# Kernel tuning notes

Measured on AMD Instinct MI355X. Metric: run time of the kernel, lower is better.

The kernel has to match this reference:

```python
import jax, jax.numpy as jnp
import numpy as np

N, E, IN_DIM, HID, OUT = 50000, 800000, 128, 64, 64


def setup_inputs() -> dict:
    key = jax.random.key(0)
    ks = jax.random.split(key, 8)
    x = jax.random.normal(ks[0], (N, IN_DIM), dtype=jnp.float32)
    edge_index = jax.random.randint(ks[1], (2, E), 0, N, dtype=jnp.int64)
    # Glorot-style init like PyG GCNConv linear; bias zeros-init equivalent -> small randn for generality
    def glorot(k, fan_in, fan_out):
        s = (6.0 / (fan_in + fan_out)) ** 0.5
        return jax.random.uniform(k, (fan_in, fan_out), jnp.float32, -s, s)
    W1 = glorot(ks[2], IN_DIM, HID)
    b1 = jnp.zeros((HID,), jnp.float32)
    W2 = glorot(ks[3], HID, HID)
    b2 = jnp.zeros((HID,), jnp.float32)
    W3 = glorot(ks[4], HID, OUT)
    b3 = jnpp = jnp.zeros((OUT,), jnp.float32)
    return {"x": x, "edge_index": edge_index, "W1": W1, "b1": b1,
            "W2": W2, "b2": b2, "W3": W3, "b3": b3}


def _gcn_norm(edge_index, num_nodes):
    # PyG gcn_norm with add_self_loops=True, edge_weight=1:
    # A_hat = A + I; deg over target column; norm = d^-1/2[src] * d^-1/2[dst]
    loops = jnp.arange(num_nodes, dtype=edge_index.dtype)
    src = jnp.concatenate([edge_index[0], loops])
    dst = jnp.concatenate([edge_index[1], loops])
    ones = jnp.ones(src.shape[0], dtype=jnp.float32)
    deg = jax.ops.segment_sum(ones, dst, num_segments=num_nodes)
    dinv = jnp.where(deg > 0, jax.lax.rsqrt(deg), 0.0)
    norm = dinv[src] * dinv[dst]  # [E+N]
    return src, dst, norm


def _conv(h, src, dst, norm, W, b, num_nodes):
    h = h @ W                         # [N, F_out] dense transform first (PyG order)
    msg = norm[:, None] * h[src]      # gather + degree-normalize, [E+N, F_out]
    out = jax.ops.segment_sum(msg, dst, num_segments=num_nodes)  # scatter-add
    return out + b


def reference(x, edge_index, W1, b1, W2, b2, W3, b3):
    num_nodes = x.shape[0]
    src, dst, norm = _gcn_norm(edge_index, num_nodes)
    h = _conv(x, src, dst, norm, W1, b1, num_nodes)
    h = jax.nn.relu(h)  # dropout is identity in eval / p=0
    h = _conv(h, src, dst, norm, W2, b2, num_nodes)
    h = jax.nn.relu(h)
    h = _conv(h, src, dst, norm, W3, b3, num_nodes)
    return h
```

## Files before the change

### kernel.cpp

```cpp
#include <hip/hip_runtime.h>


#define FD 64
#define P1CHUNK 4096
#define CAP 8192

typedef unsigned short ushort_t;
typedef unsigned int uint_t;

__device__ __forceinline__ ushort_t f2bf(float f) {
    uint_t u = __float_as_uint(f);
    u = (u + 0x7fffu + ((u >> 16) & 1u)) >> 16;
    return (ushort_t)u;
}
__device__ __forceinline__ uint_t pack2bf(float f0, float f1) {
    return (uint_t)f2bf(f0) | ((uint_t)f2bf(f1) << 16);
}

__global__ __launch_bounds__(256) void scan_buckets(const int* __restrict__ cnt,
                                                    int* __restrict__ bucketBase,
                                                    int* __restrict__ rowptr,
                                                    int NB, int N, int E) {
    __shared__ int wsum[4];
    int tid = threadIdx.x, lane = tid & 63, wv = tid >> 6;
    int v = (tid < NB) ? min(cnt[tid], CAP) : 0;
    int x = v;
    for (int off = 1; off < 64; off <<= 1) {
        int t = __shfl_up(x, off, 64);
        if (lane >= off) x += t;
    }
    if (lane == 63) wsum[wv] = x;
    __syncthreads();
    int wex = 0;
    for (int i = 0; i < wv; ++i) wex += wsum[i];
    int excl = wex + x - v;
    if (tid < NB) bucketBase[tid] = excl;
    if (tid == 0) { bucketBase[NB] = E; rowptr[N] = E; }
}

template <int K, bool SCALE>
__device__ __forceinline__ void gemm_body(int bid, const float* __restrict__ x,
                                          const float* __restrict__ W,
                                          const float* __restrict__ dinv,
                                          ushort_t* __restrict__ out, int nrows,
                                          float* Xs ) {
    constexpr int KP = K + 4;
    constexpr int NC = K / 4;
    constexpr int YP = 68;
    const int tid = threadIdx.x;
    const int lane = tid & 63;
    const int rowBase = bid * 64;

    for (int idx = tid; idx < 64 * NC; idx += 256) {
        int row = idx / NC, kc = idx % NC;
        int r = rowBase + row;
        float4 v = (r < nrows) ? *(const float4*)(x + (size_t)r * K + kc * 4)
                               : make_float4(0.f, 0.f, 0.f, 0.f);
        *(float4*)(&Xs[row * KP + kc * 4]) = v;
    }
    __syncthreads();

    const int c0 = __builtin_amdgcn_readfirstlane((tid >> 6) * 16);
    float acc[16];
#pragma unroll
    for (int i = 0; i < 16; ++i) acc[i] = 0.f;
    const float* Xrow = &Xs[lane * KP];

#pragma unroll 4
    for (int k = 0; k < K; k += 4) {
        float4 xv = *(const float4*)(Xrow + k);
        const float* wp = W + (size_t)k * FD + c0;
#pragma unroll
        for (int ci = 0; ci < 16; ++ci) {
            acc[ci] = fmaf(xv.x, wp[ci], acc[ci]);
            acc[ci] = fmaf(xv.y, wp[FD + ci], acc[ci]);
            acc[ci] = fmaf(xv.z, wp[2 * FD + ci], acc[ci]);
            acc[ci] = fmaf(xv.w, wp[3 * FD + ci], acc[ci]);
        }
    }

    int r = rowBase + lane;
    float di = 1.0f;
    if (SCALE) di = (r < nrows) ? dinv[r] : 0.f;
    __syncthreads();
    float* Ys = Xs;
#pragma unroll
    for (int ci = 0; ci < 16; ++ci) Ys[lane * YP + c0 + ci] = acc[ci] * di;
    __syncthreads();

    for (int i = tid; i < 64 * 16; i += 256) {
        int row = i >> 4, seg = i & 15;
        int rr = rowBase + row;
        if (rr < nrows) {
            float4 v = *(const float4*)(&Ys[row * YP + seg * 4]);
            uint2 p;
            p.x = pack2bf(v.x, v.y);
            p.y = pack2bf(v.z, v.w);
            *(uint2*)(out + (size_t)rr * FD + seg * 4) = p;
        }
    }
}

template <int K>
__global__ __launch_bounds__(256) void gemm_kernel(const float* __restrict__ x,
                                                   const float* __restrict__ W,
                                                   const float* __restrict__ dinv,
                                                   ushort_t* __restrict__ out, int nrows) {
    __shared__ float Xs[64 * (K + 4)];
    gemm_body<K, true>(blockIdx.x, x, W, dinv, out, nrows, Xs);
}

__global__ __launch_bounds__(256) void fused_gemm1_scatter(
    const float* __restrict__ x, const float* __restrict__ W1,
    ushort_t* __restrict__ hB, int nrows,
    const int* __restrict__ src, const int* __restrict__ dst,
    int* __restrict__ cnt, uint_t* __restrict__ staged, int E, int nGemmBlk) {
    __shared__ float Xs[64 * 132];
    int bid = blockIdx.x;
    if (bid < nGemmBlk) {
        gemm_body<128, false>(bid, x, W1, nullptr, hB, nrows, Xs);
        return;
    }
    int* hist = (int*)Xs;
    int* gbase = hist + 256;
    int tid = threadIdx.x;
    hist[tid] = 0;
    __syncthreads();
    int base = (bid - nGemmBlk) * P1CHUNK;
#pragma unroll
    for (int k = 0; k < 16; ++k) {
        int e = base + k * 256 + tid;
        if (e < E) atomicAdd(&hist[dst[e] >> 8], 1);
    }
    __syncthreads();
    int h = hist[tid];
    gbase[tid] = h ? atomicAdd(&cnt[tid], h) : 0;
    hist[tid] = 0;
    __syncthreads();
#pragma unroll
    for (int k = 0; k < 16; ++k) {
        int e = base + k * 256 + tid;
        if (e < E) {
            int s = src[e], d = dst[e];
            int b = d >> 8;
            int r = atomicAdd(&hist[b], 1);
            int p = gbase[b] + r;
            if (p < CAP) staged[(size_t)b * CAP + p] = (uint_t)s | ((uint_t)(d & 255) << 16);
        }
    }
}

__global__ __launch_bounds__(256) void bucket_sort(const uint_t* __restrict__ staged,
                                                   const int* __restrict__ cnt,
                                                   const int* __restrict__ bucketBase,
                                                   int* __restrict__ rowptr,
                                                   float* __restrict__ dinv,
                                                   ushort_t* __restrict__ csr,
                                                   ushort_t* __restrict__ hB,
                                                   int* __restrict__ dhist, int N) {
    __shared__ int ncnt[256];
    __shared__ int nrp[256];
    __shared__ int wsum[4];
    __shared__ float sdinv[256];
    __shared__ int dh[64];
    int tid = threadIdx.x, lane = tid & 63, wv = tid >> 6;
    int b = blockIdx.x;
    int gbeg = bucketBase[b];
    int cntE = min(cnt[b], CAP);
    const uint_t* sb = staged + (size_t)b * CAP;
    ncnt[tid] = 0;
    if (tid < 64) dh[tid] = 0;
    __syncthreads();
    for (int i = tid; i < cntE; i += 256)
        atomicAdd(&ncnt[(sb[i] >> 16) & 255], 1);
    __syncthreads();
    int v = ncnt[tid];
    int x = v;
    for (int off = 1; off < 64; off <<= 1) {
        int t = __shfl_up(x, off, 64);
        if (lane >= off) x += t;
    }
    if (lane == 63) wsum[wv] = x;
    __syncthreads();
    int wex = 0;
    for (int i = 0; i < wv; ++i) wex += wsum[i];
    int excl = wex + x - v;
    nrp[tid] = excl;
    int node = b * 256 + tid;
    float di = rsqrtf((float)(v + 1));
    sdinv[tid] = di;
    if (node < N) {
        dinv[node] = di;
        atomicAdd(&dh[min(v, 63)], 1);
    }
    if (node <= N) rowptr[node] = gbeg + excl;
    ncnt[tid] = 0;
    __syncthreads();
    if (tid < 64 && dh[tid]) atomicAdd(&dhist[tid], dh[tid]);
    for (int i = tid; i < cntE; i += 256) {
        uint_t p = sb[i];
        int dl = (p >> 16) & 255;
        int lofs = atomicAdd(&ncnt[dl], 1);
        csr[(size_t)gbeg + nrp[dl] + lofs] = (ushort_t)(p & 0xffffu);
    }
    uint2* hB2 = (uint2*)hB;
    for (int idx = tid; idx < 256 * 16; idx += 256) {
        int row = idx >> 4, c = idx & 15;
        int g = b * 256 + row;
        if (g < N) {
            float d = sdinv[row];
            uint2 u = hB2[(size_t)g * 16 + c];
            float f0 = __uint_as_float(u.x << 16) * d;
            float f1 = __uint_as_float(u.x & 0xffff0000u) * d;
            float f2 = __uint_as_float(u.y << 16) * d;
            float f3 = __uint_as_float(u.y & 0xffff0000u) * d;
            uint2 o;
            o.x = pack2bf(f0, f1);
            o.y = pack2bf(f2, f3);
            hB2[(size_t)g * 16 + c] = o;
        }
    }
}

__global__ void deg_scan(const int* __restrict__ dhist, int* __restrict__ dcursor) {
    int lane = threadIdx.x;
    int v = dhist[lane];
    int x = v;
    for (int off = 1; off < 64; off <<= 1) {
        int t = __shfl_up(x, off, 64);
        if (lane >= off) x += t;
    }
    dcursor[lane] = x - v;
}

__global__ __launch_bounds__(256) void deg_scatter(const int* __restrict__ rowptr,
                                                   int* __restrict__ dcursor,
                                                   int* __restrict__ perm, int N) {
    __shared__ int h[64];
    __shared__ int gb[64];
    int tid = threadIdx.x;
    if (tid < 64) h[tid] = 0;
    __syncthreads();
    int node = blockIdx.x * 256 + tid;
    bool val = node < N;
    int d = 0;
    if (val) {
        d = min(rowptr[node + 1] - rowptr[node], 63);
        atomicAdd(&h[d], 1);
    }
    __syncthreads();
    if (tid < 64) {
        int c = h[tid];
        gb[tid] = c ? atomicAdd(&dcursor[tid], c) : 0;
        h[tid] = 0;
    }
    __syncthreads();
    if (val) {
        int r = atomicAdd(&h[d], 1);
        perm[gb[d] + r] = node;
    }
}

__device__ __forceinline__ void bf8_acc(uint4 a, float* acc) {
    acc[0] += __uint_as_float(a.x << 16);
    acc[1] += __uint_as_float(a.x & 0xffff0000u);
    acc[2] += __uint_as_float(a.y << 16);
    acc[3] += __uint_as_float(a.y & 0xffff0000u);
    acc[4] += __uint_as_float(a.z << 16);
    acc[5] += __uint_as_float(a.z & 0xffff0000u);
    acc[6] += __uint_as_float(a.w << 16);
    acc[7] += __uint_as_float(a.w & 0xffff0000u);
}

template <bool RELU>
__global__ __launch_bounds__(256) void agg_fused(
    const int* __restrict__ rowptr, const ushort_t* __restrict__ csr,
    const int* __restrict__ perm,
    const float* __restrict__ dinv, const ushort_t* __restrict__ h,
    const float* __restrict__ b, float* __restrict__ out, int N) {
    int wid = (blockIdx.x * blockDim.x + threadIdx.x) >> 6;
    int lane = threadIdx.x & 63;
    int l8 = lane & 7;
    int widx = wid * 8 + (lane >> 3);
    bool valid = widx < N;
    int nd = perm[valid ? widx : 0];
    int beg = rowptr[nd];
    int end = valid ? rowptr[nd + 1] : beg;
    const uint4* __restrict__ h4 = (const uint4*)h;
    float acc[8];
#pragma unroll
    for (int k = 0; k < 8; ++k) acc[k] = 0.f;
    bf8_acc(h4[(size_t)nd * 8 + l8], acc);
    int j = beg;
    for (; j + 3 < end; j += 4) {
        int s0 = csr[j], s1 = csr[j + 1], s2 = csr[j + 2], s3 = csr[j + 3];
        uint4 a0 = h4[(size_t)s0 * 8 + l8];
        uint4 a1 = h4[(size_t)s1 * 8 + l8];
        uint4 a2 = h4[(size_t)s2 * 8 + l8];
        uint4 a3 = h4[(size_t)s3 * 8 + l8];
        bf8_acc(a0, acc); bf8_acc(a1, acc); bf8_acc(a2, acc); bf8_acc(a3, acc);
    }
    for (; j < end; ++j) bf8_acc(h4[(size_t)csr[j] * 8 + l8], acc);

    float di = dinv[nd];
    float4 b0 = *(const float4*)(b + l8 * 8);
    float4 b1 = *(const float4*)(b + l8 * 8 + 4);
    float4 v0, v1;
    v0.x = fmaf(di, acc[0], b0.x); v0.y = fmaf(di, acc[1], b0.y);
    v0.z = fmaf(di, acc[2], b0.z); v0.w = fmaf(di, acc[3], b0.w);
    v1.x = fmaf(di, acc[4], b1.x); v1.y = fmaf(di, acc[5], b1.y);
    v1.z = fmaf(di, acc[6], b1.z); v1.w = fmaf(di, acc[7], b1.w);
    if (RELU) {
        v0.x = fmaxf(v0.x, 0.f); v0.y = fmaxf(v0.y, 0.f);
        v0.z = fmaxf(v0.z, 0.f); v0.w = fmaxf(v0.w, 0.f);
        v1.x = fmaxf(v1.x, 0.f); v1.y = fmaxf(v1.y, 0.f);
        v1.z = fmaxf(v1.z, 0.f); v1.w = fmaxf(v1.w, 0.f);
    }
    if (valid) {
        float* op = out + (size_t)nd * FD + l8 * 8;
        *(float4*)op = v0;
        *(float4*)(op + 4) = v1;
    }
}

extern "C" void kernel_launch(void* const* d_in, const int* in_sizes, int n_in,
                              void* d_out, int out_size, void* d_ws, size_t ws_size,
                              hipStream_t stream) {
    const float* x  = (const float*)d_in[0];
    const int*   ei = (const int*)d_in[1];
    const float* W1 = (const float*)d_in[2];
    const float* b1 = (const float*)d_in[3];
    const float* W2 = (const float*)d_in[4];
    const float* b2 = (const float*)d_in[5];
    const float* W3 = (const float*)d_in[6];
    const float* b3 = (const float*)d_in[7];
    float* out = (float*)d_out;

    const int N = in_sizes[0] / 128;
    const int E = in_sizes[1] / 2;
    const int* src = ei;
    const int* dst = ei + E;
    const int NB = (N + 255) / 256;

    float*    f1     = (float*)d_ws;
    ushort_t* hB     = (ushort_t*)(f1 + (size_t)N * FD);
    float*    dinv   = (float*)(hB + (size_t)N * FD);
    int*      rowptr = (int*)(dinv + N);
    int*   cnt       = rowptr + N + 1;
    int*   dhist     = cnt + NB;
    int*   dcursor   = dhist + 64;
    int*   bucketBase= dcursor + 64;
    int*   perm      = bucketBase + NB + 1;
    uint_t*   staged = (uint_t*)(perm + N);
    ushort_t* csr    = (ushort_t*)(staged + (size_t)NB * CAP);

    const int nSctBlk = (E + P1CHUNK - 1) / P1CHUNK;
    const int nGemmBlk = (N + 63) / 64;
    dim3 blk(256);
    dim3 gGemm(nGemmBlk);
    dim3 gAgg((N + 31) / 32);

    hipMemsetAsync(cnt, 0, (size_t)(NB + 64) * sizeof(int), stream);
    fused_gemm1_scatter<<<dim3(nGemmBlk + nSctBlk), blk, 0, stream>>>(
        x, W1, hB, N, src, dst, cnt, staged, E, nGemmBlk);
    scan_buckets<<<dim3(1), blk, 0, stream>>>(cnt, bucketBase, rowptr, NB, N, E);
    bucket_sort<<<dim3(NB), blk, 0, stream>>>(staged, cnt, bucketBase, rowptr, dinv,
                                              csr, hB, dhist, N);
    deg_scan<<<dim3(1), dim3(64), 0, stream>>>(dhist, dcursor);
    deg_scatter<<<dim3(NB), blk, 0, stream>>>(rowptr, dcursor, perm, N);

    agg_fused<true><<<gAgg, blk, 0, stream>>>(rowptr, csr, perm, dinv, hB, b1, f1, N);

    gemm_kernel<64><<<gGemm, blk, 0, stream>>>(f1, W2, dinv, hB, N);
    agg_fused<true><<<gAgg, blk, 0, stream>>>(rowptr, csr, perm, dinv, hB, b2, f1, N);

    gemm_kernel<64><<<gGemm, blk, 0, stream>>>(f1, W3, dinv, hB, N);
    agg_fused<false><<<gAgg, blk, 0, stream>>>(rowptr, csr, perm, dinv, hB, b3, out, N);
}
```

Before: 141.1 us.

## Fuse layer aggregation with next-layer dense transform into single kernel

Aggregation for layers 1 and 2 now runs in one 512-thread kernel per layer. It applies bias and ReLU, stages the 64 aggregated rows in shared memory, multiplies them by the next weight matrix, scales by dinv, and writes bf16 output directly. This removes the fp32 intermediate round-trip through global memory and two separate GEMM launches. Rows in a block follow the degree-sorted permutation, so the output writes are scattered, and ping-pong bf16 buffers replace the fp32 workspace.

```diff
diff --git a/kernel.cpp b/kernel.cpp
--- a/kernel.cpp
+++ b/kernel.cpp
@@ -38,15 +38,11 @@
     if (tid == 0) { bucketBase[NB] = E; rowptr[N] = E; }
 }
 
-template <int K, bool SCALE>
-__device__ __forceinline__ void gemm_body(int bid, const float* __restrict__ x,
-                                          const float* __restrict__ W,
-                                          const float* __restrict__ dinv,
-                                          ushort_t* __restrict__ out, int nrows,
-                                          float* Xs ) {
-    constexpr int KP = K + 4;
-    constexpr int NC = K / 4;
-    constexpr int YP = 68;
+__device__ __forceinline__ void gemm_body128(int bid, const float* __restrict__ x,
+                                             const float* __restrict__ W,
+                                             ushort_t* __restrict__ out, int nrows,
+                                             float* Xs ) {
+    constexpr int K = 128, KP = 132, NC = 32, YP = 68;
     const int tid = threadIdx.x;
     const int lane = tid & 63;
     const int rowBase = bid * 64;
@@ -78,14 +74,10 @@
             acc[ci] = fmaf(xv.w, wp[3 * FD + ci], acc[ci]);
         }
     }
-
-    int r = rowBase + lane;
-    float di = 1.0f;
-    if (SCALE) di = (r < nrows) ? dinv[r] : 0.f;
     __syncthreads();
     float* Ys = Xs;
 #pragma unroll
-    for (int ci = 0; ci < 16; ++ci) Ys[lane * YP + c0 + ci] = acc[ci] * di;
+    for (int ci = 0; ci < 16; ++ci) Ys[lane * YP + c0 + ci] = acc[ci];
     __syncthreads();
 
     for (int i = tid; i < 64 * 16; i += 256) {
@@ -101,15 +93,6 @@
     }
 }
 
-template <int K>
-__global__ __launch_bounds__(256) void gemm_kernel(const float* __restrict__ x,
-                                                   const float* __restrict__ W,
-                                                   const float* __restrict__ dinv,
-                                                   ushort_t* __restrict__ out, int nrows) {
-    __shared__ float Xs[64 * (K + 4)];
-    gemm_body<K, true>(blockIdx.x, x, W, dinv, out, nrows, Xs);
-}
-
 __global__ __launch_bounds__(256) void fused_gemm1_scatter(
     const float* __restrict__ x, const float* __restrict__ W1,
     ushort_t* __restrict__ hB, int nrows,
@@ -118,7 +101,7 @@
     __shared__ float Xs[64 * 132];
     int bid = blockIdx.x;
     if (bid < nGemmBlk) {
-        gemm_body<128, false>(bid, x, W1, nullptr, hB, nrows, Xs);
+        gemm_body128(bid, x, W1, hB, nrows, Xs);
         return;
     }
     int* hist = (int*)Xs;
@@ -272,8 +255,84 @@
     acc[7] += __uint_as_float(a.w & 0xffff0000u);
 }
 
-template <bool RELU>
-__global__ __launch_bounds__(256) void agg_fused(
+__global__ __launch_bounds__(512) void agg_gemm(
+    const int* __restrict__ rowptr, const ushort_t* __restrict__ csr,
+    const int* __restrict__ perm, const float* __restrict__ dinv,
+    const ushort_t* __restrict__ hIn, const float* __restrict__ bias,
+    const float* __restrict__ W, ushort_t* __restrict__ hOut, int N) {
+    __shared__ float Xs[64 * 65];
+    __shared__ float sdi[64];
+    __shared__ int snode[64];
+    const int tid = threadIdx.x;
+    const int wave = tid >> 6, lane = tid & 63;
+    const int l8 = lane & 7;
+    const int nodeSlot = wave * 8 + (lane >> 3);
+    int widx = blockIdx.x * 64 + nodeSlot;
+    bool valid = widx < N;
+    int nd = perm[valid ? widx : 0];
+    int beg = rowptr[nd];
+    int end = valid ? rowptr[nd + 1] : beg;
+    const uint4* __restrict__ h4 = (const uint4*)hIn;
+    float acc[8];
+#pragma unroll
+    for (int k = 0; k < 8; ++k) acc[k] = 0.f;
+    bf8_acc(h4[(size_t)nd * 8 + l8], acc);
+    int j = beg;
+    for (; j + 3 < end; j += 4) {
+        int s0 = csr[j], s1 = csr[j + 1], s2 = csr[j + 2], s3 = csr[j + 3];
+        uint4 a0 = h4[(size_t)s0 * 8 + l8];
+        uint4 a1 = h4[(size_t)s1 * 8 + l8];
+        uint4 a2 = h4[(size_t)s2 * 8 + l8];
+        uint4 a3 = h4[(size_t)s3 * 8 + l8];
+        bf8_acc(a0, acc); bf8_acc(a1, acc); bf8_acc(a2, acc); bf8_acc(a3, acc);
+    }
+    for (; j < end; ++j) bf8_acc(h4[(size_t)csr[j] * 8 + l8], acc);
+
+    float di = dinv[nd];
+    const float* bp = bias + l8 * 8;
+    if (l8 == 0) { sdi[nodeSlot] = di; snode[nodeSlot] = valid ? nd : -1; }
+#pragma unroll
+    for (int k = 0; k < 8; ++k) {
+        float v = fmaf(di, acc[k], bp[k]);
+        v = fmaxf(v, 0.f);
+        Xs[nodeSlot * 65 + l8 * 8 + k] = v;
+    }
+    __syncthreads();
+
+    const int c0 = __builtin_amdgcn_readfirstlane(wave * 8);
+    float a2[8];
+#pragma unroll
+    for (int i = 0; i < 8; ++i) a2[i] = 0.f;
+    const float* Xrow = &Xs[lane * 65];
+#pragma unroll 4
+    for (int k = 0; k < 64; ++k) {
+        float xv = Xrow[k];
+        const float* wp = W + k * FD + c0;
+#pragma unroll
+        for (int ci = 0; ci < 8; ++ci) a2[ci] = fmaf(xv, wp[ci], a2[ci]);
+    }
+    float dro = sdi[lane];
+    int gnode = snode[lane];
+    (void)gnode;
+    __syncthreads();
+#pragma unroll
+    for (int ci = 0; ci < 8; ++ci) Xs[lane * 65 + c0 + ci] = a2[ci] * dro;
+    __syncthreads();
+
+    for (int i = tid; i < 64 * 16; i += 512) {
+        int row = i >> 4, seg = i & 15;
+        int g = snode[row];
+        if (g >= 0) {
+            const float* yp = &Xs[row * 65 + seg * 4];
+            uint2 p;
+            p.x = pack2bf(yp[0], yp[1]);
+            p.y = pack2bf(yp[2], yp[3]);
+            *(uint2*)(hOut + (size_t)g * FD + seg * 4) = p;
+        }
+    }
+}
+
+__global__ __launch_bounds__(256) void agg_final(
     const int* __restrict__ rowptr, const ushort_t* __restrict__ csr,
     const int* __restrict__ perm,
     const float* __restrict__ dinv, const ushort_t* __restrict__ h,
@@ -310,12 +369,6 @@
     v0.z = fmaf(di, acc[2], b0.z); v0.w = fmaf(di, acc[3], b0.w);
     v1.x = fmaf(di, acc[4], b1.x); v1.y = fmaf(di, acc[5], b1.y);
     v1.z = fmaf(di, acc[6], b1.z); v1.w = fmaf(di, acc[7], b1.w);
-    if (RELU) {
-        v0.x = fmaxf(v0.x, 0.f); v0.y = fmaxf(v0.y, 0.f);
-        v0.z = fmaxf(v0.z, 0.f); v0.w = fmaxf(v0.w, 0.f);
-        v1.x = fmaxf(v1.x, 0.f); v1.y = fmaxf(v1.y, 0.f);
-        v1.z = fmaxf(v1.z, 0.f); v1.w = fmaxf(v1.w, 0.f);
-    }
     if (valid) {
         float* op = out + (size_t)nd * FD + l8 * 8;
         *(float4*)op = v0;
@@ -342,9 +395,9 @@
     const int* dst = ei + E;
     const int NB = (N + 255) / 256;
 
-    float*    f1     = (float*)d_ws;
-    ushort_t* hB     = (ushort_t*)(f1 + (size_t)N * FD);
-    float*    dinv   = (float*)(hB + (size_t)N * FD);
+    ushort_t* hB     = (ushort_t*)d_ws;
+    ushort_t* hB2    = hB + (size_t)N * FD;
+    float*    dinv   = (float*)(hB2 + (size_t)N * FD);
     int*      rowptr = (int*)(dinv + N);
     int*   cnt       = rowptr + N + 1;
     int*   dhist     = cnt + NB;
@@ -357,8 +410,6 @@
     const int nSctBlk = (E + P1CHUNK - 1) / P1CHUNK;
     const int nGemmBlk = (N + 63) / 64;
     dim3 blk(256);
-    dim3 gGemm(nGemmBlk);
-    dim3 gAgg((N + 31) / 32);
 
     hipMemsetAsync(cnt, 0, (size_t)(NB + 64) * sizeof(int), stream);
     fused_gemm1_scatter<<<dim3(nGemmBlk + nSctBlk), blk, 0, stream>>>(
@@ -369,11 +420,10 @@
     deg_scan<<<dim3(1), dim3(64), 0, stream>>>(dhist, dcursor);
     deg_scatter<<<dim3(NB), blk, 0, stream>>>(rowptr, dcursor, perm, N);
 
-    agg_fused<true><<<gAgg, blk, 0, stream>>>(rowptr, csr, perm, dinv, hB, b1, f1, N);
-
-    gemm_kernel<64><<<gGemm, blk, 0, stream>>>(f1, W2, dinv, hB, N);
-    agg_fused<true><<<gAgg, blk, 0, stream>>>(rowptr, csr, perm, dinv, hB, b2, f1, N);
-
-    gemm_kernel<64><<<gGemm, blk, 0, stream>>>(f1, W3, dinv, hB, N);
-    agg_fused<false><<<gAgg, blk, 0, stream>>>(rowptr, csr, perm, dinv, hB, b3, out, N);
-}
+    agg_gemm<<<dim3(nGemmBlk), dim3(512), 0, stream>>>(
+        rowptr, csr, perm, dinv, hB, b1, W2, hB2, N);
+    agg_gemm<<<dim3(nGemmBlk), dim3(512), 0, stream>>>(
+        rowptr, csr, perm, dinv, hB2, b2, W3, hB, N);
+    agg_final<<<dim3((N + 31) / 32), blk, 0, stream>>>(
+        rowptr, csr, perm, dinv, hB, b3, out, N);
+}
```

Result: faster. 120.8 us (-14.4%).
